# Performance work log

Measured on AMD Instinct MI355X. Metric: run time of the kernel, lower is better.

The kernel has to match this reference:

```python
import jax, jax.numpy as jnp
import numpy as np

B, N, FEAT, HID, CTX = 16384, 7, 512, 256, 256
COMB = N * HID + CTX  # 2048


def setup_inputs() -> dict:
    key = jax.random.key(0)
    ks = jax.random.split(key, 20)
    s = lambda k, shape, sc=0.05: jax.random.normal(k, shape, dtype=jnp.float32) * sc
    adj = jax.random.randint(ks[1], (N, N), 0, 2).astype(jnp.float32)
    # guarantee self-loops so no row is fully masked (still exercise nan_to_num path robustly)
    adj = jnp.maximum(adj, jnp.eye(N, dtype=jnp.float32))
    return {
        "node_feats": jax.random.normal(ks[0], (B, N, FEAT), dtype=jnp.float32),
        "adj": adj,
        "context": jax.random.normal(ks[2], (B, CTX), dtype=jnp.float32),
        "base_preds": jax.random.normal(ks[3], (B, 5), dtype=jnp.float32),
        "W1": s(ks[4], (HID, FEAT)),
        "a1": s(ks[5], (1, 2 * HID)),
        "W2": s(ks[6], (HID, HID)),
        "a2": s(ks[7], (1, 2 * HID)),
        "wh1_w": s(ks[8], (32, COMB)), "wh1_b": s(ks[9], (32,)),
        "wh2_w": s(ks[10], (16, 32)), "wh2_b": s(ks[11], (16,)),
        "wh3_w": s(ks[12], (5, 16)), "wh3_b": s(ks[13], (5,)),
        "rh1_w": s(ks[14], (16, COMB)), "rh1_b": s(ks[15], (16,)),
        "rh2_w": s(ks[16], (1, 16)), "rh2_b": s(ks[17], (1,)),
    }


def _gat_layer(x, adj, W, a):
    # x: (B, N, in_dim); W: (D, in_dim); a: (1, 2D)
    h = jnp.einsum('bni,di->bnd', x, W)  # (B, N, D)
    D = W.shape[0]
    # a([h_i, h_j]) == h_i @ a[:, :D] + h_j @ a[:, D:]
    s_i = h @ a[0, :D]   # (B, N)
    s_j = h @ a[0, D:]   # (B, N)
    e = s_i[:, :, None] + s_j[:, None, :]          # (B, N, N)
    e = jax.nn.leaky_relu(e, negative_slope=0.2)
    e = jnp.where(adj[None] == 0, -jnp.inf, e)
    alpha = jax.nn.softmax(e, axis=-1)
    alpha = jnp.nan_to_num(alpha, nan=0.0)
    out = jnp.einsum('bij,bjd->bid', alpha, h)     # (B, N, D)
    return out, alpha


def reference(node_feats, adj, context, base_preds, W1, a1, W2, a2,
              wh1_w, wh1_b, wh2_w, wh2_b, wh3_w, wh3_b,
              rh1_w, rh1_b, rh2_w, rh2_b):
    h, _attn1 = _gat_layer(node_feats, adj, W1, a1)
    h = jax.nn.relu(h)
    h, attn2 = _gat_layer(h, adj, W2, a2)
    h = jax.nn.relu(h)
    graph_embed = h.reshape(h.shape[0], -1)                 # (B, N*D)
    combined = jnp.concatenate([graph_embed, context], -1)  # (B, COMB)
    # weight head (dropout is inference-mode identity)
    t = jax.nn.relu(combined @ wh1_w.T + wh1_b)
    t = jax.nn.relu(t @ wh2_w.T + wh2_b)
    raw_weights = t @ wh3_w.T + wh3_b                       # (B, 5)
    weights = jax.nn.softmax(raw_weights, axis=-1)
    weighted_pred = jnp.sum(weights * base_preds, axis=-1)  # (B,)
    r = jnp.tanh(combined @ rh1_w.T + rh1_b)
    residual = (r @ rh2_w.T + rh2_b)[:, 0] * 0.05
    pred = jnp.maximum(weighted_pred + residual, 0.05)
    return pred, weights, attn2
```

## Files before the change

kernel.cpp:

```cpp
#include <hip/hip_runtime.h>

#define B_SZ 16384
#define NN 7
#define HID 256
#define COMB 2048

typedef __attribute__((ext_vector_type(8))) short short8;
typedef __attribute__((ext_vector_type(4))) float floatx4;
typedef __attribute__((ext_vector_type(4))) unsigned short ushortx4;
typedef unsigned short us;

__device__ __forceinline__ float bf2f(us u) {
    union { unsigned int i; float f; } v; v.i = ((unsigned int)u) << 16; return v.f;
}
__device__ __forceinline__ us f2bf(float f) {
    union { unsigned int i; float f; } v; v.f = f;
    return (us)((v.i + 0x7FFFu + ((v.i >> 16) & 1u)) >> 16);
}
__device__ __forceinline__ us f2bf_fast(float f) {
    union { unsigned int i; float f; } v; v.f = f;
    return (us)((v.i + 0x8000u) >> 16);
}
__device__ __forceinline__ void gl_lds16(const us* g, us* l) {
    __builtin_amdgcn_global_load_lds(
        (const __attribute__((address_space(1))) unsigned int*)g,
        (__attribute__((address_space(3))) unsigned int*)l, 16, 0, 0);
}

__global__ __launch_bounds__(256) void pack_weights(const float* __restrict__ W1,
                                                    const float* __restrict__ W2,
                                                    const float* __restrict__ wh1,
                                                    const float* __restrict__ rh1,
                                                    us* __restrict__ dst) {
    int i = (blockIdx.x * 256 + threadIdx.x) * 4;
    if (i >= 294912) return;
    const float* src; int off;
    if (i < 131072)      { src = W1;  off = i; }
    else if (i < 196608) { src = W2;  off = i - 131072; }
    else if (i < 262144) { src = wh1; off = i - 196608; }
    else                 { src = rh1; off = i - 262144; }
    floatx4 v = *(const floatx4*)(src + off);
    ushortx4 o = {f2bf(v[0]), f2bf(v[1]), f2bf(v[2]), f2bf(v[3])};
    *(ushortx4*)(dst + i) = o;
}

template <int SRC_STRIDE, bool WRITE_ALPHA>
__device__ __forceinline__ void attn_graph(const us* hb, const float* adjs, const float* avec,
                                           us* dst, int dstStride, float* alpha_dst, int lane) {
    float hv[NN][4];
#pragma unroll
    for (int n = 0; n < NN; ++n) {
        ushortx4 r = *(const ushortx4*)(hb + n * SRC_STRIDE + lane * 4);
        hv[n][0] = bf2f(r[0]); hv[n][1] = bf2f(r[1]);
        hv[n][2] = bf2f(r[2]); hv[n][3] = bf2f(r[3]);
    }
    floatx4 ai = *(const floatx4*)(avec + lane * 4);
    floatx4 aj = *(const floatx4*)(avec + HID + lane * 4);
    float si[NN], sj[NN];
#pragma unroll
    for (int n = 0; n < NN; ++n) {
        float pi = hv[n][0] * ai[0] + hv[n][1] * ai[1] + hv[n][2] * ai[2] + hv[n][3] * ai[3];
        float pj = hv[n][0] * aj[0] + hv[n][1] * aj[1] + hv[n][2] * aj[2] + hv[n][3] * aj[3];
#pragma unroll
        for (int off = 32; off; off >>= 1) {
            pi += __shfl_xor(pi, off);
            pj += __shfl_xor(pj, off);
        }
        si[n] = pi; sj[n] = pj;
    }
    const int j = lane & 7;
    float sjm = sj[0];
    if (j == 1) sjm = sj[1];
    if (j == 2) sjm = sj[2];
    if (j == 3) sjm = sj[3];
    if (j == 4) sjm = sj[4];
    if (j == 5) sjm = sj[5];
    if (j == 6) sjm = sj[6];
    const int jc = (j < 7) ? j : 0;
    float alpha[NN];
#pragma unroll
    for (int i = 0; i < NN; ++i) {
        float x = si[i] + sjm;
        x = (x >= 0.f) ? x : 0.2f * x;
        bool ok = (j < 7) && (adjs[i * 7 + jc] != 0.f);
        float e = ok ? x : -1e30f;
        float m = e;
        m = fmaxf(m, __shfl_xor(m, 1, 8));
        m = fmaxf(m, __shfl_xor(m, 2, 8));
        m = fmaxf(m, __shfl_xor(m, 4, 8));
        float ex = ok ? __expf(e - m) : 0.f;
        float s = ex;
        s += __shfl_xor(s, 1, 8);
        s += __shfl_xor(s, 2, 8);
        s += __shfl_xor(s, 4, 8);
        alpha[i] = (s > 0.f) ? ex * __frcp_rn(s) : 0.f;
    }
    if (WRITE_ALPHA && lane < 7) {
#pragma unroll
        for (int i = 0; i < NN; ++i) alpha_dst[i * NN + lane] = alpha[i];
    }
#pragma unroll
    for (int i = 0; i < NN; ++i) {
        floatx4 o = (floatx4){0.f, 0.f, 0.f, 0.f};
#pragma unroll
        for (int jj = 0; jj < NN; ++jj) {
            float a = __shfl(alpha[i], jj, 8);
            o[0] += a * hv[jj][0]; o[1] += a * hv[jj][1];
            o[2] += a * hv[jj][2]; o[3] += a * hv[jj][3];
        }
        ushortx4 st = {f2bf(fmaxf(o[0], 0.f)), f2bf(fmaxf(o[1], 0.f)),
                       f2bf(fmaxf(o[2], 0.f)), f2bf(fmaxf(o[3], 0.f))};
        *(ushortx4*)(dst + i * dstStride + lane * 4) = st;
    }
}


__global__ __launch_bounds__(512, 4) void fused_g1(const float* __restrict__ Af,
                                                   const us* __restrict__ W1b,
                                                   const float* __restrict__ adj,
                                                   const float* __restrict__ avec,
                                                   us* __restrict__ x2g) {
    __shared__ __attribute__((aligned(16))) us As[4096];
    __shared__ __attribute__((aligned(16))) us hs[56 * 264];
    __shared__ float adjs[52];
    const int tid = threadIdx.x;
    const int wave = tid >> 6, lane = tid & 63;
    const int quad = lane >> 4, m16 = lane & 15;
    const long rowBase = (long)blockIdx.x * 56;
    if (tid < 49) adjs[tid] = adj[tid];

    floatx4 acc[4][2];
#pragma unroll
    for (int rt = 0; rt < 4; ++rt)
#pragma unroll
        for (int ct = 0; ct < 2; ++ct) acc[rt][ct] = (floatx4){0.f, 0.f, 0.f, 0.f};

    const int r = tid >> 3, kq8 = tid & 7;
    long rowA = rowBase + r; if (rowA > 114687) rowA = 114687;
    const float* aptr = Af + rowA * 512 + kq8 * 8;
    us* wdst = &As[((r >> 3) * 64 + (r & 7) * 8 + kq8) * 8];
    const int colb = wave * 32;

    for (int s = 0; s < 8; ++s) {
        const int k0 = s * 64;
        floatx4 v0 = *(const floatx4*)(aptr + k0);
        floatx4 v1 = *(const floatx4*)(aptr + k0 + 4);
        short8 sv;
        sv[0] = f2bf_fast(v0[0]); sv[1] = f2bf_fast(v0[1]);
        sv[2] = f2bf_fast(v0[2]); sv[3] = f2bf_fast(v0[3]);
        sv[4] = f2bf_fast(v1[0]); sv[5] = f2bf_fast(v1[1]);
        sv[6] = f2bf_fast(v1[2]); sv[7] = f2bf_fast(v1[3]);
        *(short8*)wdst = sv;
        __syncthreads();
#pragma unroll
        for (int t = 0; t < 2; ++t) {
            short8 b0 = *(const short8*)(W1b + (long)(colb + m16) * 512 + k0 + t * 32 + quad * 8);
            short8 b1 = *(const short8*)(W1b + (long)(colb + 16 + m16) * 512 + k0 + t * 32 + quad * 8);
            short8 a[4];
#pragma unroll
            for (int rt = 0; rt < 4; ++rt)
                a[rt] = *(const short8*)&As[((rt * 2 + (m16 >> 3)) * 64 + (m16 & 7) * 8 + t * 4 + quad) * 8];
#pragma unroll
            for (int rt = 0; rt < 4; ++rt) {
                acc[rt][0] = __builtin_amdgcn_mfma_f32_16x16x32_bf16(a[rt], b0, acc[rt][0], 0, 0, 0);
                acc[rt][1] = __builtin_amdgcn_mfma_f32_16x16x32_bf16(a[rt], b1, acc[rt][1], 0, 0, 0);
            }
        }
        __syncthreads();
    }
#pragma unroll
    for (int rt = 0; rt < 4; ++rt)
#pragma unroll
        for (int ct = 0; ct < 2; ++ct)
#pragma unroll
            for (int i = 0; i < 4; ++i) {
                int row = rt * 16 + quad * 4 + i;
                if (row < 56) hs[row * 264 + wave * 32 + ct * 16 + m16] = f2bf(acc[rt][ct][i]);
            }
    __syncthreads();
    attn_graph<264, false>(&hs[wave * 7 * 264], adjs, avec,
                           x2g + ((long)blockIdx.x * 64 + wave * 7) * 256, 256, nullptr, lane);
}

__global__ __launch_bounds__(512, 4) void fused_rest(const us* __restrict__ x2g,
                                                     const us* __restrict__ W2b,
                                                     const us* __restrict__ Whb,
                                                     const float* __restrict__ adj,
                                                     const float* __restrict__ avec,
                                                     const float* __restrict__ context,
                                                     const float* __restrict__ wh1_b,
                                                     const float* __restrict__ wh2_w,
                                                     const float* __restrict__ wh2_b,
                                                     const float* __restrict__ wh3_w,
                                                     const float* __restrict__ wh3_b,
                                                     const float* __restrict__ rh1_b,
                                                     const float* __restrict__ rh2_w,
                                                     const float* __restrict__ rh2_b,
                                                     const float* __restrict__ base_preds,
                                                     float* __restrict__ out) {
    __shared__ __attribute__((aligned(16))) us As[4096];
    __shared__ __attribute__((aligned(16))) us hs[56 * 264];
    __shared__ __attribute__((aligned(16))) us ctxs[8 * 264];
    __shared__ float red[8 * 384];
    __shared__ float fin[384];
    __shared__ float adjs[52];
    const int tid = threadIdx.x;
    const int wave = tid >> 6, lane = tid & 63;
    const int quad = lane >> 4, m16 = lane & 15;
    const long rowBaseX = (long)blockIdx.x * 64;
    const long gbase = (long)blockIdx.x * 8;
    if (tid < 49) adjs[tid] = adj[tid];
    {
        int cr = tid >> 6, c4 = (tid & 63) * 4;
        floatx4 cv = *(const floatx4*)(context + (gbase + cr) * 256 + c4);
        ushortx4 st = {f2bf(cv[0]), f2bf(cv[1]), f2bf(cv[2]), f2bf(cv[3])};
        *(ushortx4*)&ctxs[cr * 264 + c4] = st;
    }

    floatx4 acc[4][2];
#pragma unroll
    for (int rt = 0; rt < 4; ++rt)
#pragma unroll
        for (int ct = 0; ct < 2; ++ct) acc[rt][ct] = (floatx4){0.f, 0.f, 0.f, 0.f};
    const int colb = wave * 32;

    for (int s = 0; s < 4; ++s) {
        const int k0 = s * 64;
        gl_lds16(x2g + (rowBaseX + wave * 8 + (lane >> 3)) * 256 + k0 + (lane & 7) * 8,
                 &As[wave * 512]);
        __syncthreads();
#pragma unroll
        for (int t = 0; t < 2; ++t) {
            short8 b0 = *(const short8*)(W2b + (long)(colb + m16) * 256 + k0 + t * 32 + quad * 8);
            short8 b1 = *(const short8*)(W2b + (long)(colb + 16 + m16) * 256 + k0 + t * 32 + quad * 8);
            short8 a[4];
#pragma unroll
            for (int rt = 0; rt < 4; ++rt)
                a[rt] = *(const short8*)&As[((rt * 2 + (m16 >> 3)) * 64 + (m16 & 7) * 8 + t * 4 + quad) * 8];
#pragma unroll
            for (int rt = 0; rt < 4; ++rt) {
                acc[rt][0] = __builtin_amdgcn_mfma_f32_16x16x32_bf16(a[rt], b0, acc[rt][0], 0, 0, 0);
                acc[rt][1] = __builtin_amdgcn_mfma_f32_16x16x32_bf16(a[rt], b1, acc[rt][1], 0, 0, 0);
            }
        }
        __syncthreads();
    }
#pragma unroll
    for (int rt = 0; rt < 4; ++rt)
#pragma unroll
        for (int ct = 0; ct < 2; ++ct)
#pragma unroll
            for (int i = 0; i < 4; ++i) {
                int row = rt * 16 + quad * 4 + i;
                if (row < 56) hs[row * 264 + wave * 32 + ct * 16 + m16] = f2bf(acc[rt][ct][i]);
            }
    __syncthreads();
    float* alf = out + 6 * B_SZ;
    attn_graph<264, true>(&hs[wave * 7 * 264], adjs, avec,
                          &hs[wave * 7 * 264], 264, alf + (gbase + wave) * 49, lane);
    __syncthreads();
    floatx4 acc3[3];
#pragma unroll
    for (int ct = 0; ct < 3; ++ct) acc3[ct] = (floatx4){0.f, 0.f, 0.f, 0.f};
    const int g = m16 & 7;
#pragma unroll
    for (int s2 = 0; s2 < 8; ++s2) {
        const int kk = s2 * 32;
        short8 a;
        if (wave < 7) a = *(const short8*)&hs[(g * 7 + wave) * 264 + kk + quad * 8];
        else          a = *(const short8*)&ctxs[g * 264 + kk + quad * 8];
#pragma unroll
        for (int ct = 0; ct < 3; ++ct) {
            short8 bh = *(const short8*)(Whb + (long)(ct * 16 + m16) * COMB + wave * 256 + kk + quad * 8);
            acc3[ct] = __builtin_amdgcn_mfma_f32_16x16x32_bf16(a, bh, acc3[ct], 0, 0, 0);
        }
    }
#pragma unroll
    for (int ct = 0; ct < 3; ++ct)
#pragma unroll
        for (int i = 0; i < 4; ++i) {
            int g2 = quad * 4 + i;
            if (g2 < 8) red[wave * 384 + g2 * 48 + ct * 16 + m16] = acc3[ct][i];
        }
    __syncthreads();
    if (tid < 384) {
        float ssum = 0.f;
#pragma unroll
        for (int w = 0; w < 8; ++w) ssum += red[w * 384 + tid];
        fin[tid] = ssum;
    }
    __syncthreads();
    if (tid < 8) {
        const long b = gbase + tid;
        const float* g48 = &fin[tid * 48];
        float t1[32], r1[16];
#pragma unroll
        for (int k = 0; k < 32; ++k) t1[k] = fmaxf(g48[k] + wh1_b[k], 0.f);
#pragma unroll
        for (int k = 0; k < 16; ++k) r1[k] = tanhf(g48[32 + k] + rh1_b[k]);
        float t2[16];
#pragma unroll
        for (int jj = 0; jj < 16; ++jj) {
            float s = wh2_b[jj];
            for (int k = 0; k < 32; ++k) s += wh2_w[jj * 32 + k] * t1[k];
            t2[jj] = fmaxf(s, 0.f);
        }
        float rw[5], m = -1e30f;
#pragma unroll
        for (int o = 0; o < 5; ++o) {
            float s = wh3_b[o];
            for (int jj = 0; jj < 16; ++jj) s += wh3_w[o * 16 + jj] * t2[jj];
            rw[o] = s; m = fmaxf(m, s);
        }
        float se = 0.f;
#pragma unroll
        for (int o = 0; o < 5; ++o) { rw[o] = __expf(rw[o] - m); se += rw[o]; }
        float inv = 1.f / se, wp = 0.f;
#pragma unroll
        for (int o = 0; o < 5; ++o) {
            float w = rw[o] * inv;
            out[B_SZ + b * 5 + o] = w;
            wp += w * base_preds[b * 5 + o];
        }
        float rs = rh2_b[0];
#pragma unroll
        for (int k = 0; k < 16; ++k) rs += rh2_w[k] * r1[k];
        out[b] = fmaxf(wp + rs * 0.05f, 0.05f);
    }
}

extern "C" void kernel_launch(void* const* d_in, const int* in_sizes, int n_in,
                              void* d_out, int out_size, void* d_ws, size_t ws_size,
                              hipStream_t stream) {
    const float* node_feats = (const float*)d_in[0];
    const float* adj        = (const float*)d_in[1];
    const float* context    = (const float*)d_in[2];
    const float* base_preds = (const float*)d_in[3];
    const float* W1         = (const float*)d_in[4];
    const float* a1         = (const float*)d_in[5];
    const float* W2         = (const float*)d_in[6];
    const float* a2         = (const float*)d_in[7];
    const float* wh1_w = (const float*)d_in[8];
    const float* wh1_b = (const float*)d_in[9];
    const float* wh2_w = (const float*)d_in[10];
    const float* wh2_b = (const float*)d_in[11];
    const float* wh3_w = (const float*)d_in[12];
    const float* wh3_b = (const float*)d_in[13];
    const float* rh1_w = (const float*)d_in[14];
    const float* rh1_b = (const float*)d_in[15];
    const float* rh2_w = (const float*)d_in[16];
    const float* rh2_b = (const float*)d_in[17];
    float* out = (float*)d_out;

    char* ws = (char*)d_ws;
    const size_t X2B = (size_t)2048 * 64 * 256 * 2;
    us* x2  = (us*)ws;
    us* W1b = (us*)(ws + X2B);
    us* W2b = W1b + 131072;
    us* Whb = W2b + 65536;

    pack_weights<<<288, 256, 0, stream>>>(W1, W2, wh1_w, rh1_w, W1b);

    fused_g1<<<2048, 512, 0, stream>>>(node_feats, W1b, adj, a1, x2);

    fused_rest<<<2048, 512, 0, stream>>>(x2, W2b, Whb, adj, a2, context,
                                         wh1_b, wh2_w, wh2_b, wh3_w, wh3_b,
                                         rh1_b, rh2_w, rh2_b, base_preds, out);
}
```

Before: 540.8 us.

## Fuse both GAT layers and heads into one kernel, keeping layer-1 output in LDS

Merges fused_g1 and fused_rest into a single kernel. The first GAT layer's output stays in shared memory and feeds the second GEMM directly, with no bf16 round trip through a global workspace. Shared memory is aliased (As/red/fin) into one buffer, and launch bounds are raised to 6 blocks per CU for more occupancy. The cost is a single longer kernel with more register pressure and an extra barrier, and the second GEMM now reads A from a padded hs layout instead of the swizzled As.

Result: no change. 543.9 us (+0.6%).

```diff
diff --git a/kernel.cpp b/kernel.cpp
--- a/kernel.cpp
+++ b/kernel.cpp
@@ -20,11 +20,6 @@
 __device__ __forceinline__ us f2bf_fast(float f) {
     union { unsigned int i; float f; } v; v.f = f;
     return (us)((v.i + 0x8000u) >> 16);
-}
-__device__ __forceinline__ void gl_lds16(const us* g, us* l) {
-    __builtin_amdgcn_global_load_lds(
-        (const __attribute__((address_space(1))) unsigned int*)g,
-        (__attribute__((address_space(3))) unsigned int*)l, 16, 0, 0);
 }
 
 __global__ __launch_bounds__(256) void pack_weights(const float* __restrict__ W1,
@@ -114,20 +109,44 @@
     }
 }
 
-
-__global__ __launch_bounds__(512, 4) void fused_g1(const float* __restrict__ Af,
-                                                   const us* __restrict__ W1b,
-                                                   const float* __restrict__ adj,
-                                                   const float* __restrict__ avec,
-                                                   us* __restrict__ x2g) {
-    __shared__ __attribute__((aligned(16))) us As[4096];
-    __shared__ __attribute__((aligned(16))) us hs[56 * 264];
-    __shared__ float adjs[52];
+__global__ __launch_bounds__(512, 6) void fused_all(const float* __restrict__ Af,
+                                                    const us* __restrict__ W1b,
+                                                    const us* __restrict__ W2b,
+                                                    const us* __restrict__ Whb,
+                                                    const float* __restrict__ adj,
+                                                    const float* __restrict__ a1,
+                                                    const float* __restrict__ a2,
+                                                    const float* __restrict__ context,
+                                                    const float* __restrict__ wh1_b,
+                                                    const float* __restrict__ wh2_w,
+                                                    const float* __restrict__ wh2_b,
+                                                    const float* __restrict__ wh3_w,
+                                                    const float* __restrict__ wh3_b,
+                                                    const float* __restrict__ rh1_b,
+                                                    const float* __restrict__ rh2_w,
+                                                    const float* __restrict__ rh2_b,
+                                                    const float* __restrict__ base_preds,
+                                                    float* __restrict__ out) {
+    __shared__ __attribute__((aligned(16))) char smem[52036];
+    us* As = (us*)smem;
+    float* red = (float*)smem;
+    float* fin = (float*)(smem + 12288);
+    us* hs = (us*)(smem + 13824);
+    us* ctxs = (us*)(smem + 47616);
+    float* adjs = (float*)(smem + 51840);
+
     const int tid = threadIdx.x;
     const int wave = tid >> 6, lane = tid & 63;
     const int quad = lane >> 4, m16 = lane & 15;
     const long rowBase = (long)blockIdx.x * 56;
+    const long gbase = (long)blockIdx.x * 8;
     if (tid < 49) adjs[tid] = adj[tid];
+    {
+        int cr = tid >> 6, c4 = (tid & 63) * 4;
+        floatx4 cv = *(const floatx4*)(context + (gbase + cr) * 256 + c4);
+        ushortx4 st = {f2bf(cv[0]), f2bf(cv[1]), f2bf(cv[2]), f2bf(cv[3])};
+        *(ushortx4*)&ctxs[cr * 264 + c4] = st;
+    }
 
     floatx4 acc[4][2];
 #pragma unroll
@@ -178,73 +197,30 @@
                 if (row < 56) hs[row * 264 + wave * 32 + ct * 16 + m16] = f2bf(acc[rt][ct][i]);
             }
     __syncthreads();
-    attn_graph<264, false>(&hs[wave * 7 * 264], adjs, avec,
-                           x2g + ((long)blockIdx.x * 64 + wave * 7) * 256, 256, nullptr, lane);
-}
-
-__global__ __launch_bounds__(512, 4) void fused_rest(const us* __restrict__ x2g,
-                                                     const us* __restrict__ W2b,
-                                                     const us* __restrict__ Whb,
-                                                     const float* __restrict__ adj,
-                                                     const float* __restrict__ avec,
-                                                     const float* __restrict__ context,
-                                                     const float* __restrict__ wh1_b,
-                                                     const float* __restrict__ wh2_w,
-                                                     const float* __restrict__ wh2_b,
-                                                     const float* __restrict__ wh3_w,
-                                                     const float* __restrict__ wh3_b,
-                                                     const float* __restrict__ rh1_b,
-                                                     const float* __restrict__ rh2_w,
-                                                     const float* __restrict__ rh2_b,
-                                                     const float* __restrict__ base_preds,
-                                                     float* __restrict__ out) {
-    __shared__ __attribute__((aligned(16))) us As[4096];
-    __shared__ __attribute__((aligned(16))) us hs[56 * 264];
-    __shared__ __attribute__((aligned(16))) us ctxs[8 * 264];
-    __shared__ float red[8 * 384];
-    __shared__ float fin[384];
-    __shared__ float adjs[52];
-    const int tid = threadIdx.x;
-    const int wave = tid >> 6, lane = tid & 63;
-    const int quad = lane >> 4, m16 = lane & 15;
-    const long rowBaseX = (long)blockIdx.x * 64;
-    const long gbase = (long)blockIdx.x * 8;
-    if (tid < 49) adjs[tid] = adj[tid];
-    {
-        int cr = tid >> 6, c4 = (tid & 63) * 4;
-        floatx4 cv = *(const floatx4*)(context + (gbase + cr) * 256 + c4);
-        ushortx4 st = {f2bf(cv[0]), f2bf(cv[1]), f2bf(cv[2]), f2bf(cv[3])};
-        *(ushortx4*)&ctxs[cr * 264 + c4] = st;
-    }
-
-    floatx4 acc[4][2];
+
+    attn_graph<264, false>(&hs[wave * 7 * 264], adjs, a1, &hs[wave * 7 * 264], 264, nullptr, lane);
+    __syncthreads();
+
 #pragma unroll
     for (int rt = 0; rt < 4; ++rt)
 #pragma unroll
         for (int ct = 0; ct < 2; ++ct) acc[rt][ct] = (floatx4){0.f, 0.f, 0.f, 0.f};
-    const int colb = wave * 32;
-
-    for (int s = 0; s < 4; ++s) {
-        const int k0 = s * 64;
-        gl_lds16(x2g + (rowBaseX + wave * 8 + (lane >> 3)) * 256 + k0 + (lane & 7) * 8,
-                 &As[wave * 512]);
-        __syncthreads();
-#pragma unroll
-        for (int t = 0; t < 2; ++t) {
-            short8 b0 = *(const short8*)(W2b + (long)(colb + m16) * 256 + k0 + t * 32 + quad * 8);
-            short8 b1 = *(const short8*)(W2b + (long)(colb + 16 + m16) * 256 + k0 + t * 32 + quad * 8);
-            short8 a[4];
-#pragma unroll
-            for (int rt = 0; rt < 4; ++rt)
-                a[rt] = *(const short8*)&As[((rt * 2 + (m16 >> 3)) * 64 + (m16 & 7) * 8 + t * 4 + quad) * 8];
-#pragma unroll
-            for (int rt = 0; rt < 4; ++rt) {
-                acc[rt][0] = __builtin_amdgcn_mfma_f32_16x16x32_bf16(a[rt], b0, acc[rt][0], 0, 0, 0);
-                acc[rt][1] = __builtin_amdgcn_mfma_f32_16x16x32_bf16(a[rt], b1, acc[rt][1], 0, 0, 0);
-            }
-        }
-        __syncthreads();
-    }
+#pragma unroll
+    for (int ks = 0; ks < 8; ++ks) {
+        const int kk = ks * 32;
+        short8 b0 = *(const short8*)(W2b + (long)(colb + m16) * 256 + kk + quad * 8);
+        short8 b1 = *(const short8*)(W2b + (long)(colb + 16 + m16) * 256 + kk + quad * 8);
+        short8 a[4];
+#pragma unroll
+        for (int rt = 0; rt < 4; ++rt)
+            a[rt] = *(const short8*)&hs[(rt * 16 + m16) * 264 + kk + quad * 8];
+#pragma unroll
+        for (int rt = 0; rt < 4; ++rt) {
+            acc[rt][0] = __builtin_amdgcn_mfma_f32_16x16x32_bf16(a[rt], b0, acc[rt][0], 0, 0, 0);
+            acc[rt][1] = __builtin_amdgcn_mfma_f32_16x16x32_bf16(a[rt], b1, acc[rt][1], 0, 0, 0);
+        }
+    }
+    __syncthreads();
 #pragma unroll
     for (int rt = 0; rt < 4; ++rt)
 #pragma unroll
@@ -255,10 +231,12 @@
                 if (row < 56) hs[row * 264 + wave * 32 + ct * 16 + m16] = f2bf(acc[rt][ct][i]);
             }
     __syncthreads();
+
     float* alf = out + 6 * B_SZ;
-    attn_graph<264, true>(&hs[wave * 7 * 264], adjs, avec,
-                          &hs[wave * 7 * 264], 264, alf + (gbase + wave) * 49, lane);
-    __syncthreads();
+    attn_graph<264, true>(&hs[wave * 7 * 264], adjs, a2, &hs[wave * 7 * 264], 264,
+                          alf + (gbase + wave) * 49, lane);
+    __syncthreads();
+
     floatx4 acc3[3];
 #pragma unroll
     for (int ct = 0; ct < 3; ++ct) acc3[ct] = (floatx4){0.f, 0.f, 0.f, 0.f};
@@ -275,6 +253,7 @@
             acc3[ct] = __builtin_amdgcn_mfma_f32_16x16x32_bf16(a, bh, acc3[ct], 0, 0, 0);
         }
     }
+    __syncthreads();
 #pragma unroll
     for (int ct = 0; ct < 3; ++ct)
 #pragma unroll
@@ -352,18 +331,13 @@
     const float* rh2_b = (const float*)d_in[17];
     float* out = (float*)d_out;
 
-    char* ws = (char*)d_ws;
-    const size_t X2B = (size_t)2048 * 64 * 256 * 2;
-    us* x2  = (us*)ws;
-    us* W1b = (us*)(ws + X2B);
+    us* W1b = (us*)d_ws;
     us* W2b = W1b + 131072;
     us* Whb = W2b + 65536;
 
     pack_weights<<<288, 256, 0, stream>>>(W1, W2, wh1_w, rh1_w, W1b);
 
-    fused_g1<<<2048, 512, 0, stream>>>(node_feats, W1b, adj, a1, x2);
-
-    fused_rest<<<2048, 512, 0, stream>>>(x2, W2b, Whb, adj, a2, context,
-                                         wh1_b, wh2_w, wh2_b, wh3_w, wh3_b,
-                                         rh1_b, rh2_w, rh2_b, base_preds, out);
-}
+    fused_all<<<2048, 512, 0, stream>>>(node_feats, W1b, W2b, Whb, adj, a1, a2, context,
+                                        wh1_b, wh2_w, wh2_b, wh3_w, wh3_b,
+                                        rh1_b, rh2_w, rh2_b, base_preds, out);
+}
```
